# Kernel optimization log

Measured on AMD Instinct MI355X. Metric: run time of the kernel, lower is better.

The kernel has to match this reference:

```python
import jax, jax.numpy as jnp
import numpy as np
from jax import lax

D = 30   # embedding_dim (hardcoded in repo)
Q = 30   # question length
N = 4000 # number of sentences in doc
S = 100  # tokens per sentence
K = 5    # k_for_maxpool
SLOPE = 0.1  # LeakyReLU negative slope


def setup_inputs() -> dict:
    key = jax.random.key(0)
    ks = jax.random.split(key, 20)
    rn = lambda k, sh: jax.random.normal(k, sh, dtype=jnp.float32)
    ru = lambda k, sh: jax.random.uniform(k, sh, dtype=jnp.float32)
    return {
        "doc_sents_embeds": rn(ks[0], (N, S, D)),
        "sents_gaf": ru(ks[1], (N, 3)),
        "question_embeds": rn(ks[2], (Q, D)),
        "q_idfs": ru(ks[3], (Q, 1)),
        "doc_gaf": ru(ks[4], (4,)),
        "conv1_w": rn(ks[5], (D, D, 3)) * 0.1,
        "conv1_b": rn(ks[6], (D,)) * 0.1,
        "conv2_w": rn(ks[7], (D, D, 3)) * 0.1,
        "conv2_b": rn(ks[8], (D,)) * 0.1,
        "qw_W": rn(ks[9], (1, D + 1)) * 0.1,
        "qw_b": rn(ks[10], (1,)) * 0.1,
        "lq1_W": rn(ks[11], (8, 6)) * 0.1,
        "lq1_b": rn(ks[12], (8,)) * 0.1,
        "lq2_W": rn(ks[13], (1, 8)) * 0.1,
        "lq2_b": rn(ks[14], (1,)) * 0.1,
        "so_W": rn(ks[15], (1, 4)) * 0.1,
        "so_b": rn(ks[16], (1,)) * 0.1,
        "fl_W": rn(ks[17], (1, 5)) * 0.1,
        "fl_b": rn(ks[18], (1,)) * 0.1,
    }


def _leaky(x):
    return jnp.where(x >= 0, x, SLOPE * x)


def _conv_block(x, w, b):
    # x: [B, L, D]. torch Conv1d(D, D, 3, padding=2) then slice [1:L+1]
    # is exactly a 'same' conv with padding 1 on each side; then residual add.
    y = lax.conv_general_dilated(x.transpose(0, 2, 1), w, (1,), [(1, 1)],
                                 dimension_numbers=("NCH", "OIH", "NCH"))
    y = _leaky(y + b[None, :, None])
    return y.transpose(0, 2, 1) + x


def _cos_sim(A, B):
    # A: [Q, D], B: [N, S, D] -> [N, Q, S] (num/den as in torch my_cosine_sim)
    num = jnp.einsum("qd,nsd->nqs", A, B)
    den = jnp.linalg.norm(A, axis=-1)[None, :, None] * jnp.linalg.norm(B, axis=-1)[:, None, :]
    return num / den


def _pool(sim):
    # sort-based k-max pooling -> [max, avg_of_top_k]; sim: [N, Q, S] -> [N, Q, 2]
    vals = lax.top_k(sim, K)[0]  # descending
    return jnp.stack([vals[..., 0], vals.mean(-1)], axis=-1)


def reference(doc_sents_embeds, sents_gaf, question_embeds, q_idfs, doc_gaf,
              conv1_w, conv1_b, conv2_w, conv2_b, qw_W, qw_b,
              lq1_W, lq1_b, lq2_W, lq2_b, so_W, so_b, fl_W, fl_b):
    # question context (two residual trigram convs)
    q_conv = _conv_block(question_embeds[None], conv1_w, conv1_b)
    q_conv = _conv_block(q_conv, conv2_w, conv2_b)[0]          # [Q, D]
    # question term weights
    qw_in = jnp.concatenate([q_conv, q_idfs], axis=-1)          # [Q, D+1]
    q_weights = jax.nn.softmax((qw_in @ qw_W.T + qw_b)[:, 0])   # [Q]
    # sentence context convs (batched over all sentences)
    conv_res = _conv_block(doc_sents_embeds, conv1_w, conv1_b)
    conv_res = _conv_block(conv_res, conv2_w, conv2_b)          # [N, S, D]
    # similarity matrices
    sim_insens = _cos_sim(question_embeds, doc_sents_embeds)    # [N, Q, S]
    sim_oh = (sim_insens > 1.0 - 1e-3).astype(sim_insens.dtype)
    sim_sens = _cos_sim(q_conv, conv_res)
    # k-max pooling and per-q tiny MLP attention
    feats = jnp.concatenate([_pool(sim_oh), _pool(sim_insens), _pool(sim_sens)], axis=-1)  # [N, Q, 6]
    lo = _leaky(feats @ lq1_W.T + lq1_b) @ lq2_W.T + lq2_b      # [N, Q, 1]
    lo = lo[..., 0] * q_weights[None, :]
    sent_emit = lo.sum(-1) / Q                                  # [N]
    # per-sentence output layer
    sent_feats = jnp.concatenate([sents_gaf, sent_emit[:, None]], axis=-1)  # [N, 4]
    sent_scores = jax.nn.sigmoid((sent_feats @ so_W.T + so_b)[:, 0])        # [N]
    # doc-level score
    doc_rep = jnp.concatenate([jnp.max(sent_scores)[None], doc_gaf])        # [5]
    final = doc_rep @ fl_W.T + fl_b                                          # [1]
    return final, sent_scores
```

## Files before the change

kernel.cpp:

```cpp
#include <hip/hip_runtime.h>
#include <hip/hip_bf16.h>

#define SLOPE 0.1f

#define OFF_QW    1816
#define OFF_QNI   1846
#define OFF_QNS   1876
#define OFF_QNN   1906
#define OFF_B1    4606
#define OFF_B2    7336
#define OFF_LQ1W  7366
#define OFF_LQ1B  7414
#define OFF_LQ2W  7422
#define OFF_LQ2B  7430
#define OFF_SOW   7431
#define OFF_SOB   7435
#define OFF_FLW   7436
#define OFF_FLB   7441
#define U16_QEA   16384
#define U16_QCA   17408
#define U16_WB1   18432
#define U16_WB2   21504

typedef __attribute__((ext_vector_type(8))) __bf16 bf16x8;
typedef __attribute__((ext_vector_type(4))) float f32x4;

union Frag { uint4 u4; uint u[4]; bf16x8 v; };

__device__ __forceinline__ float bf2f(ushort h) {
    union { uint u; float f; } c; c.u = ((uint)h) << 16; return c.f;
}
__device__ __forceinline__ ushort f2bf(float f) {
    union { float f; uint u; } c; c.f = f;
    uint u = c.u;
    return (ushort)((u + 0x7FFFu + ((u >> 16) & 1u)) >> 16);
}
__device__ __forceinline__ float ldx(const void* p, long i, int bf) {
    if (bf) return bf2f(((const ushort*)p)[i]);
    return ((const float*)p)[i];
}
__device__ __forceinline__ uint pk2(float lo, float hi) {
    uint r;
    asm("v_cvt_pk_bf16_f32 %0, %1, %2" : "=v"(r) : "v"(lo), "v"(hi));
    return r;
}
__device__ __forceinline__ float blo(uint u) { return __uint_as_float(u << 16); }
__device__ __forceinline__ float bhi(uint u) { return __uint_as_float(u & 0xFFFF0000u); }
__device__ __forceinline__ float lk(float x) { return fmaxf(x, SLOPE * x); }

#define LGKM0() asm volatile("s_waitcnt lgkmcnt(0)" ::: "memory")

#define CE(x, y) { float _hi = fmaxf(x, y), _lo = fminf(x, y); x = _hi; y = _lo; }

__device__ __forceinline__ void sort4d(float& a, float& b, float& c, float& d) {
    CE(a, b); CE(c, d); CE(a, c); CE(b, d); CE(b, c);
}
__device__ __forceinline__ void merge44_5(const float* a, const float* b, float* t) {
    t[0] = fmaxf(a[0], b[0]);
    t[1] = fmaxf(fminf(a[0], b[0]), fmaxf(a[1], b[1]));
    t[2] = fmaxf(fmaxf(fminf(a[0], b[1]), fminf(a[1], b[0])), fmaxf(a[2], b[2]));
    t[3] = fmaxf(fmaxf(fminf(a[0], b[2]), fminf(a[1], b[1])),
                 fmaxf(fminf(a[2], b[0]), fmaxf(a[3], b[3])));
    t[4] = fmaxf(fmaxf(fminf(a[0], b[3]), fminf(a[1], b[2])),
                 fmaxf(fminf(a[2], b[1]), fminf(a[3], b[0])));
}
__device__ __forceinline__ void merge54_5(const float* a, const float* b, float* t) {
    t[0] = fmaxf(a[0], b[0]);
    t[1] = fmaxf(fminf(a[0], b[0]), fmaxf(a[1], b[1]));
    t[2] = fmaxf(fmaxf(fminf(a[0], b[1]), fminf(a[1], b[0])), fmaxf(a[2], b[2]));
    t[3] = fmaxf(fmaxf(fminf(a[0], b[2]), fminf(a[1], b[1])),
                 fmaxf(fminf(a[2], b[0]), fmaxf(a[3], b[3])));
    t[4] = fmaxf(fmaxf(fmaxf(fminf(a[0], b[3]), fminf(a[1], b[2])),
                       fmaxf(fminf(a[2], b[1]), fminf(a[3], b[0]))), a[4]);
}
__device__ __forceinline__ void merge55_5(const float* a, const float* b, float* t) {
    t[0] = fmaxf(a[0], b[0]);
    t[1] = fmaxf(fminf(a[0], b[0]), fmaxf(a[1], b[1]));
    t[2] = fmaxf(fmaxf(fminf(a[0], b[1]), fminf(a[1], b[0])), fmaxf(a[2], b[2]));
    t[3] = fmaxf(fmaxf(fminf(a[0], b[2]), fminf(a[1], b[1])),
                 fmaxf(fminf(a[2], b[0]), fmaxf(a[3], b[3])));
    t[4] = fmaxf(fmaxf(fmaxf(fminf(a[0], b[3]), fminf(a[1], b[2])),
                       fmaxf(fminf(a[2], b[1]), fminf(a[3], b[0]))),
                 fmaxf(a[4], b[4]));
}

__device__ __forceinline__ int detect_bf(const void* doc_in, int tid, int* scnt) {
    if (tid == 0) *scnt = 0;
    __syncthreads();
    const ushort* p = (const ushort*)doc_in;
    int local = 0;
    for (int i = tid; i < 4096; i += 256) {
        unsigned e = (p[i] >> 7) & 0xFFu;
        if (e != 0u && (e < 100u || e > 134u)) local++;
    }
    atomicAdd(scnt, local);
    __syncthreads();
    return (*scnt > 200) ? 0 : 1;
}

__global__ __launch_bounds__(256) void k_prep(
        const void* doc_in,
        const void* qe_in, const void* qidf_in,
        const void* w1_in, const void* b1_in,
        const void* w2_in, const void* b2_in,
        const void* qwW_in, const void* qwb_in,
        const void* lq1W_in, const void* lq1b_in,
        const void* lq2W_in, const void* lq2b_in,
        const void* soW_in, const void* sob_in,
        const void* flW_in, const void* flb_in,
        float* ws) {
    const int tid = threadIdx.x;
    const int blk = blockIdx.x;
    __shared__ float QE[900], T1[900], QC[900], W[2700], IDF[32], LG[32];
    __shared__ int scnt;

    const int bf = detect_bf(doc_in, tid, &scnt);
    ushort* wsu = (ushort*)ws;

    if (blk == 1) {
        if (tid == 0) { ((int*)ws)[0] = bf; }
        if (tid < 30) ws[OFF_B1 + tid] = ldx(b1_in, tid, bf);
        if (tid < 48) ws[OFF_LQ1W + tid] = ldx(lq1W_in, tid, bf);
        if (tid < 8)  { ws[OFF_LQ1B + tid] = ldx(lq1b_in, tid, bf);
                        ws[OFF_LQ2W + tid] = ldx(lq2W_in, tid, bf); }
        if (tid < 4)  ws[OFF_SOW + tid] = ldx(soW_in, tid, bf);
        if (tid < 5)  ws[OFF_FLW + tid] = ldx(flW_in, tid, bf);
        if (tid == 1) { ws[OFF_LQ2B] = ldx(lq2b_in, 0, bf);
                        ws[OFF_SOB]  = ldx(sob_in, 0, bf);
                        ws[OFF_FLB]  = ldx(flb_in, 0, bf); }
        for (int i = tid; i < 3072; i += 256) {
            int o = i / 96, kk = i % 96;
            int k = kk >> 5, ii = kk & 31;
            float v1 = 0.f;
            if (o < 30 && ii < 30) v1 = ldx(w1_in, (long)o*90 + ii*3 + k, bf);
            wsu[U16_WB1 + i] = f2bf(v1);
        }
        return;
    }
    if (blk == 2) {
        if (tid < 30) ws[OFF_B2 + tid] = ldx(b2_in, tid, bf);
        for (int i = tid; i < 3072; i += 256) {
            int o = i / 96, kk = i % 96;
            int k = kk >> 5, ii = kk & 31;
            float v2 = 0.f;
            if (o < 30 && ii < 30) v2 = ldx(w2_in, (long)o*90 + ii*3 + k, bf);
            wsu[U16_WB2 + i] = f2bf(v2);
        }
        return;
    }

    if (tid == 0) { ((int*)ws)[0] = bf; }

    for (int i = tid; i < 900; i += 256) QE[i] = ldx(qe_in, i, bf);
    if (tid < 30) IDF[tid] = ldx(qidf_in, tid, bf);
    for (int i = tid; i < 2700; i += 256) W[i] = ldx(w1_in, i, bf);
    __syncthreads();

    for (int idx = tid; idx < 900; idx += 256) {
        int s = idx / 30, o = idx % 30;
        float acc = ldx(b1_in, o, bf);
        for (int k = 0; k < 3; ++k) {
            int t = s + k - 1;
            if (t < 0 || t >= 30) continue;
            for (int i = 0; i < 30; ++i) acc += QE[t*30 + i] * W[o*90 + i*3 + k];
        }
        acc = acc >= 0.f ? acc : SLOPE * acc;
        T1[idx] = acc + QE[idx];
    }
    __syncthreads();
    for (int i = tid; i < 2700; i += 256) W[i] = ldx(w2_in, i, bf);
    __syncthreads();
    for (int idx = tid; idx < 900; idx += 256) {
        int s = idx / 30, o = idx % 30;
        float acc = ldx(b2_in, o, bf);
        for (int k = 0; k < 3; ++k) {
            int t = s + k - 1;
            if (t < 0 || t >= 30) continue;
            for (int i = 0; i < 30; ++i) acc += T1[t*30 + i] * W[o*90 + i*3 + k];
        }
        acc = acc >= 0.f ? acc : SLOPE * acc;
        QC[idx] = acc + T1[idx];
    }
    __syncthreads();

    if (tid < 30) {
        float s1 = 0.f, s2 = 0.f;
        for (int d = 0; d < 30; ++d) {
            float a = QE[tid*30 + d]; s1 += a*a;
            float b = QC[tid*30 + d]; s2 += b*b;
        }
        float n1 = sqrtf(s1);
        ws[OFF_QNN + tid] = n1;
        ws[OFF_QNI + tid] = 1.0f / n1;
        ws[OFF_QNS + tid] = 1.0f / sqrtf(s2);
        float z = ldx(qwb_in, 0, bf);
        for (int d = 0; d < 30; ++d) z += QC[tid*30 + d] * ldx(qwW_in, d, bf);
        z += IDF[tid] * ldx(qwW_in, 30, bf);
        LG[tid] = z;
    }
    __syncthreads();
    if (tid == 0) {
        float m = -1e30f;
        for (int q = 0; q < 30; ++q) m = fmaxf(m, LG[q]);
        float sum = 0.f, e[30];
        for (int q = 0; q < 30; ++q) { e[q] = expf(LG[q] - m); sum += e[q]; }
        for (int q = 0; q < 30; ++q) ws[OFF_QW + q] = e[q] / sum;
    }
    for (int i = tid; i < 1024; i += 256) {
        int q = i >> 5, d = i & 31;
        float ve = (q < 30 && d < 30) ? QE[q*30 + d] : 0.f;
        float vc = (q < 30 && d < 30) ? QC[q*30 + d] : 0.f;
        wsu[U16_QEA + i] = f2bf(ve);
        wsu[U16_QCA + i] = f2bf(vc);
    }
}

__global__ __launch_bounds__(128, 5) void k_main(const void* doc_in, const void* gaf_in,
                                                 void* out, float* ws) {
    const int tid = threadIdx.x;
    const int lane = tid & 63;
    const int wid = tid >> 6;
    const int n = blockIdx.x * 2 + wid;
    const int bf = ((const int*)ws)[0];
    const int l15 = lane & 15;
    const int quad = lane >> 4;

    __shared__ __align__(16) uint Xs[2][1648];
    __shared__ __align__(16) float INVXs[2][112];
    __shared__ float FEs[2][30][6];

    uint* X = Xs[wid];
    uint4* X4 = (uint4*)X;
    float* INVX = INVXs[wid];
    float (*FE)[6] = FEs[wid];

    const ushort* wsu = (const ushort*)ws;
    const uint4* qeA = (const uint4*)(wsu + U16_QEA);
    const uint4* qcA = (const uint4*)(wsu + U16_QCA);
    const uint4* wb1 = (const uint4*)(wsu + U16_WB1);
    const uint4* wb2 = (const uint4*)(wsu + U16_WB2);

    float ga0 = ldx(gaf_in, (long)n*3 + 0, bf);
    float ga1 = ldx(gaf_in, (long)n*3 + 1, bf);
    float ga2 = ldx(gaf_in, (long)n*3 + 2, bf);

    {
        uint4 z4 = make_uint4(0u, 0u, 0u, 0u);
        if (lane < 12) X4[(lane < 4) ? lane : (400 + lane)] = z4;
        if (lane >= 12 && lane < 24) INVX[100 + (lane - 12)] = 0.f;
    }
    for (int g = lane; g < 400; g += 64) {
        int r = g >> 2, t = g & 3;
        uint4 w;
        float s2;
        if (bf) {
            const uint* gp = (const uint*)doc_in + (size_t)n * 1500 + r * 15 + t * 4;
            uint a = gp[0], b = gp[1], c = gp[2];
            uint d = (t < 3) ? gp[3] : 0u;
            w = make_uint4(a, b, c, d);
            float x0 = blo(a), x1 = bhi(a), x2 = blo(b), x3 = bhi(b);
            float x4 = blo(c), x5 = bhi(c), x6 = blo(d), x7 = bhi(d);
            s2 = x0*x0 + x1*x1 + x2*x2 + x3*x3 + x4*x4 + x5*x5 + x6*x6 + x7*x7;
        } else {
            const float* p = (const float*)doc_in + (size_t)n * 3000 + r * 30 + t * 8;
            float2 f0 = ((const float2*)p)[0];
            float2 f1 = ((const float2*)p)[1];
            float2 f2 = ((const float2*)p)[2];
            float2 f3 = (t < 3) ? ((const float2*)p)[3] : make_float2(0.f, 0.f);
            w = make_uint4(pk2(f0.x, f0.y), pk2(f1.x, f1.y), pk2(f2.x, f2.y), pk2(f3.x, f3.y));
            s2 = f0.x*f0.x + f0.y*f0.y + f1.x*f1.x + f1.y*f1.y
               + f2.x*f2.x + f2.y*f2.y + f3.x*f3.x + f3.y*f3.y;
        }
        X4[(r + 1) * 4 + t] = w;
        s2 += __shfl_xor(s2, 1);
        s2 += __shfl_xor(s2, 2);
        if (t == 0) INVX[r] = 1.f / sqrtf(s2);
    }
    LGKM0();

    auto sim_pool = [&](const uint4* qa, int iqOff, int fbase, bool do_oh, int qbase) {
        const int q = qbase + l15;
        Frag b;
        b.u4 = qa[q * 4 + quad];
        f32x4 acc[7];
        #pragma unroll
        for (int mt = 0; mt < 7; ++mt) {
            int m = mt * 16 + l15;
            Frag a;
            if (m < 100) a.u4 = X4[(m + 1) * 4 + quad];
            else         a.u4 = make_uint4(0u, 0u, 0u, 0u);
            f32x4 z = {0.f, 0.f, 0.f, 0.f};
            acc[mt] = __builtin_amdgcn_mfma_f32_16x16x32_bf16(a.v, b.v, z, 0, 0, 0);
        }
        const float4* INVX4 = (const float4*)INVX;
        float thr = (do_oh && q < 30) ? 0.999f * ws[OFF_QNN + q] : 1e30f;
        float iq  = (q < 30) ? ws[iqOff + q] : 0.f;
        float g[7][4];
        int cnt = 0;
        #pragma unroll
        for (int mt = 0; mt < 7; ++mt) {
            float4 ix = INVX4[mt * 4 + quad];
            float ixa[4] = {ix.x, ix.y, ix.z, ix.w};
            #pragma unroll
            for (int r = 0; r < 4; ++r) {
                float u = acc[mt][r] * ixa[r];
                if (mt == 6 && (quad * 4 + r) >= 4) u = -1e30f;
                g[mt][r] = u;
                if (do_oh) cnt += (u > thr) ? 1 : 0;
            }
        }
        #pragma unroll
        for (int mt = 0; mt < 7; ++mt) sort4d(g[mt][0], g[mt][1], g[mt][2], g[mt][3]);
        float p0[5], p1[5], p2[5], q0[5], q1[5], t[5];
        merge44_5(g[0], g[1], p0);
        merge44_5(g[2], g[3], p1);
        merge44_5(g[4], g[5], p2);
        merge55_5(p0, p1, q0);
        merge54_5(p2, g[6], q1);
        merge55_5(q0, q1, t);
        #pragma unroll
        for (int d = 16; d < 64; d <<= 1) {
            float pp[5];
            pp[0] = __shfl_xor(t[0], d); pp[1] = __shfl_xor(t[1], d);
            pp[2] = __shfl_xor(t[2], d); pp[3] = __shfl_xor(t[3], d);
            pp[4] = __shfl_xor(t[4], d);
            if (do_oh) cnt += __shfl_xor(cnt, d);
            float tn[5];
            merge55_5(t, pp, tn);
            t[0] = tn[0]; t[1] = tn[1]; t[2] = tn[2]; t[3] = tn[3]; t[4] = tn[4];
        }
        if (quad == 0 && q < 30) {
            if (do_oh) {
                FE[q][0] = cnt > 0 ? 1.f : 0.f;
                FE[q][1] = (float)(cnt > 5 ? 5 : cnt) * 0.2f;
            }
            FE[q][fbase]     = t[0] * iq;
            FE[q][fbase + 1] = (t[0] + t[1] + t[2] + t[3] + t[4]) * 0.2f * iq;
        }
    };

    auto conv_inplace = [&](const uint4* wb, int bOff, bool donorm) {
        Frag wf0[3], wf1[3];
        #pragma unroll
        for (int k = 0; k < 3; ++k) {
            wf0[k].u4 = wb[l15 * 12 + k * 4 + quad];
            wf1[k].u4 = wb[(16 + l15) * 12 + k * 4 + quad];
        }
        float b40[4], b41[4];
        #pragma unroll
        for (int r = 0; r < 4; ++r) {
            int o0 = quad * 4 + r, o1 = 16 + o0;
            b40[r] = ws[bOff + o0];
            b41[r] = (o1 < 30) ? ws[bOff + o1] : 0.f;
        }
        auto load_xf = [&](int mt, Frag& f0, Frag& f1, Frag& f2) {
            int s = mt * 16 + l15;
            if (s < 100) {
                f0.u4 = X4[s * 4 + quad];
                f1.u4 = X4[(s + 1) * 4 + quad];
                f2.u4 = X4[(s + 2) * 4 + quad];
            } else {
                f0.u4 = f1.u4 = f2.u4 = make_uint4(0u, 0u, 0u, 0u);
            }
        };
        Frag xf0, xf1, xf2;
        load_xf(0, xf0, xf1, xf2);
        #pragma unroll
        for (int mt = 0; mt < 7; ++mt) {
            const int s = mt * 16 + l15;
            const bool sv = (s < 100);
            const int db = (s + 1) * 16 + quad * 2;
            uint u0 = 0u, u1 = 0u, u2 = 0u, u3 = 0u;
            if (sv) {
                uint2 ua = *(const uint2*)(X + db);
                uint2 ub = *(const uint2*)(X + db + 8);
                u0 = ua.x; u1 = ua.y; u2 = ub.x; u3 = ub.y;
            }
            Frag xn0, xn1, xn2;
            if (mt < 6) load_xf(mt + 1, xn0, xn1, xn2);
            f32x4 a0 = {0.f, 0.f, 0.f, 0.f}, a1 = {0.f, 0.f, 0.f, 0.f};
            a0 = __builtin_amdgcn_mfma_f32_16x16x32_bf16(wf0[0].v, xf0.v, a0, 0, 0, 0);
            a1 = __builtin_amdgcn_mfma_f32_16x16x32_bf16(wf1[0].v, xf0.v, a1, 0, 0, 0);
            a0 = __builtin_amdgcn_mfma_f32_16x16x32_bf16(wf0[1].v, xf1.v, a0, 0, 0, 0);
            a1 = __builtin_amdgcn_mfma_f32_16x16x32_bf16(wf1[1].v, xf1.v, a1, 0, 0, 0);
            a0 = __builtin_amdgcn_mfma_f32_16x16x32_bf16(wf0[2].v, xf2.v, a0, 0, 0, 0);
            a1 = __builtin_amdgcn_mfma_f32_16x16x32_bf16(wf1[2].v, xf2.v, a1, 0, 0, 0);
            LGKM0();
            float ss = 0.f;
            if (sv) {
                float v0 = lk(a0[0] + b40[0]) + blo(u0);
                float v1 = lk(a0[1] + b40[1]) + bhi(u0);
                float v2 = lk(a0[2] + b40[2]) + blo(u1);
                float v3 = lk(a0[3] + b40[3]) + bhi(u1);
                *(uint2*)(X + db) = make_uint2(pk2(v0, v1), pk2(v2, v3));
                float w0 = lk(a1[0] + b41[0]) + blo(u2);
                float w1 = lk(a1[1] + b41[1]) + bhi(u2);
                ss = v0*v0 + v1*v1 + v2*v2 + v3*v3 + w0*w0 + w1*w1;
                if (quad < 3) {
                    float w2 = lk(a1[2] + b41[2]) + blo(u3);
                    float w3 = lk(a1[3] + b41[3]) + bhi(u3);
                    *(uint2*)(X + db + 8) = make_uint2(pk2(w0, w1), pk2(w2, w3));
                    ss += w2*w2 + w3*w3;
                } else {
                    X[db + 8] = pk2(w0, w1);
                }
            }
            if (donorm) {
                ss += __shfl_xor(ss, 16);
                ss += __shfl_xor(ss, 32);
                if (quad == 0 && sv) INVX[s] = 1.f / sqrtf(ss);
            }
            xf0 = xn0; xf1 = xn1; xf2 = xn2;
        }
    };

    sim_pool(qeA, OFF_QNI, 2, true, 0);
    sim_pool(qeA, OFF_QNI, 2, true, 16);

    conv_inplace(wb1, OFF_B1, false);
    LGKM0();
    conv_inplace(wb2, OFF_B2, true);
    LGKM0();

    sim_pool(qcA, OFF_QNS, 4, false, 0);
    sim_pool(qcA, OFF_QNS, 4, false, 16);
    LGKM0();

    float val = 0.f;
    if (lane < 30) {
        float lo = ws[OFF_LQ2B];
        #pragma unroll
        for (int j = 0; j < 8; ++j) {
            float h = ws[OFF_LQ1B + j];
            #pragma unroll
            for (int f = 0; f < 6; ++f) h += FE[lane][f] * ws[OFF_LQ1W + j*6 + f];
            h = lk(h);
            lo += h * ws[OFF_LQ2W + j];
        }
        val = lo * ws[OFF_QW + lane];
    }
    #pragma unroll
    for (int d = 32; d >= 1; d >>= 1) val += __shfl_xor(val, d);
    if (lane == 0) {
        float emit = val * (1.f / 30.f);
        float z = ws[OFF_SOB];
        z += ga0 * ws[OFF_SOW + 0];
        z += ga1 * ws[OFF_SOW + 1];
        z += ga2 * ws[OFF_SOW + 2];
        z += emit * ws[OFF_SOW + 3];
        float sc = 1.f / (1.f + expf(-z));
        if (bf) ((__hip_bfloat16*)out)[1 + n] = __float2bfloat16(sc);
        else    ((float*)out)[1 + n] = sc;
    }
}

__global__ __launch_bounds__(256) void k_final(const void* docgaf_in, void* out, const float* ws) {
    const int tid = threadIdx.x;
    const int bf = ((const int*)ws)[0];
    __shared__ float red[256];
    float m = -1e30f;
    for (int i = tid; i < 4000; i += 256) {
        float v = bf ? __bfloat162float(((const __hip_bfloat16*)out)[1 + i])
                     : ((const float*)out)[1 + i];
        m = fmaxf(m, v);
    }
    red[tid] = m;
    __syncthreads();
    for (int off = 128; off > 0; off >>= 1) {
        if (tid < off) red[tid] = fmaxf(red[tid], red[tid + off]);
        __syncthreads();
    }
    if (tid == 0) {
        float f = ws[OFF_FLB] + red[0] * ws[OFF_FLW + 0];
        for (int i = 0; i < 4; ++i) f += ldx(docgaf_in, i, bf) * ws[OFF_FLW + 1 + i];
        if (bf) ((__hip_bfloat16*)out)[0] = __float2bfloat16(f);
        else    ((float*)out)[0] = f;
    }
}

extern "C" void kernel_launch(void* const* d_in, const int* in_sizes, int n_in,
                              void* d_out, int out_size, void* d_ws, size_t ws_size,
                              hipStream_t stream) {
    float* ws = (float*)d_ws;
    k_prep<<<3, 256, 0, stream>>>(d_in[0], d_in[2], d_in[3], d_in[5], d_in[6], d_in[7], d_in[8],
                                  d_in[9], d_in[10], d_in[11], d_in[12], d_in[13], d_in[14],
                                  d_in[15], d_in[16], d_in[17], d_in[18], ws);
    k_main<<<2000, 128, 0, stream>>>(d_in[0], d_in[1], d_out, ws);
    k_final<<<1, 256, 0, stream>>>(d_in[4], d_out, ws);
}
```

Measured before the change: 179.1 us.

## Split each sentence across two waves with ping-pong LDS buffers

Changes the work mapping from one wave per sentence to two waves cooperating on one sentence: each wave handles 16 questions in the similarity/pooling stage and about half the row tiles in each conv. The in-place conv with a single buffer is replaced by ping-pong XA/XB buffers separated by __syncthreads. The row stride is packed to 15 dwords instead of 16, which turns vector LDS accesses into scalar dword loads. The aim is to halve per-wave serial latency and shrink LDS per sentence, at the cost of block barriers, a cross-wave reduction and more LDS instructions.

```diff
diff --git a/kernel.cpp b/kernel.cpp
--- a/kernel.cpp
+++ b/kernel.cpp
@@ -22,6 +22,8 @@
 #define U16_WB1   18432
 #define U16_WB2   21504
 
+#define XDW 1548
+
 typedef __attribute__((ext_vector_type(8))) __bf16 bf16x8;
 typedef __attribute__((ext_vector_type(4))) float f32x4;
 
@@ -47,8 +49,6 @@
 __device__ __forceinline__ float blo(uint u) { return __uint_as_float(u << 16); }
 __device__ __forceinline__ float bhi(uint u) { return __uint_as_float(u & 0xFFFF0000u); }
 __device__ __forceinline__ float lk(float x) { return fmaxf(x, SLOPE * x); }
-
-#define LGKM0() asm volatile("s_waitcnt lgkmcnt(0)" ::: "memory")
 
 #define CE(x, y) { float _hi = fmaxf(x, y), _lo = fminf(x, y); x = _hi; y = _lo; }
 
@@ -215,24 +215,21 @@
     }
 }
 
-__global__ __launch_bounds__(128, 5) void k_main(const void* doc_in, const void* gaf_in,
+__global__ __launch_bounds__(128, 4) void k_main(const void* doc_in, const void* gaf_in,
                                                  void* out, float* ws) {
+    const int n = blockIdx.x;
     const int tid = threadIdx.x;
+    const int bf = ((const int*)ws)[0];
     const int lane = tid & 63;
     const int wid = tid >> 6;
-    const int n = blockIdx.x * 2 + wid;
-    const int bf = ((const int*)ws)[0];
     const int l15 = lane & 15;
     const int quad = lane >> 4;
-
-    __shared__ __align__(16) uint Xs[2][1648];
-    __shared__ __align__(16) float INVXs[2][112];
-    __shared__ float FEs[2][30][6];
-
-    uint* X = Xs[wid];
-    uint4* X4 = (uint4*)X;
-    float* INVX = INVXs[wid];
-    float (*FE)[6] = FEs[wid];
+    const int q = wid * 16 + l15;
+
+    __shared__ __align__(16) uint XA[XDW];
+    __shared__ __align__(16) uint XB[XDW];
+    __shared__ __align__(16) float INVX[112];
+    __shared__ float PART[2];
 
     const ushort* wsu = (const ushort*)ws;
     const uint4* qeA = (const uint4*)(wsu + U16_QEA);
@@ -244,20 +241,22 @@
     float ga1 = ldx(gaf_in, (long)n*3 + 1, bf);
     float ga2 = ldx(gaf_in, (long)n*3 + 2, bf);
 
-    {
-        uint4 z4 = make_uint4(0u, 0u, 0u, 0u);
-        if (lane < 12) X4[(lane < 4) ? lane : (400 + lane)] = z4;
-        if (lane >= 12 && lane < 24) INVX[100 + (lane - 12)] = 0.f;
-    }
-    for (int g = lane; g < 400; g += 64) {
+    if (tid < 48) {
+        int j = (tid < 15) ? tid : (1500 + tid);
+        XA[j] = 0u; XB[j] = 0u;
+    } else if (tid < 60) {
+        INVX[100 + (tid - 48)] = 0.f;
+    }
+    for (int g = tid; g < 400; g += 128) {
         int r = g >> 2, t = g & 3;
-        uint4 w;
+        int base = (r + 1) * 15 + t * 4;
         float s2;
         if (bf) {
             const uint* gp = (const uint*)doc_in + (size_t)n * 1500 + r * 15 + t * 4;
             uint a = gp[0], b = gp[1], c = gp[2];
             uint d = (t < 3) ? gp[3] : 0u;
-            w = make_uint4(a, b, c, d);
+            XA[base] = a; XA[base + 1] = b; XA[base + 2] = c;
+            if (t < 3) XA[base + 3] = d;
             float x0 = blo(a), x1 = bhi(a), x2 = blo(b), x3 = bhi(b);
             float x4 = blo(c), x5 = bhi(c), x6 = blo(d), x7 = bhi(d);
             s2 = x0*x0 + x1*x1 + x2*x2 + x3*x3 + x4*x4 + x5*x5 + x6*x6 + x7*x7;
@@ -267,19 +266,21 @@
             float2 f1 = ((const float2*)p)[1];
             float2 f2 = ((const float2*)p)[2];
             float2 f3 = (t < 3) ? ((const float2*)p)[3] : make_float2(0.f, 0.f);
-            w = make_uint4(pk2(f0.x, f0.y), pk2(f1.x, f1.y), pk2(f2.x, f2.y), pk2(f3.x, f3.y));
+            XA[base]     = pk2(f0.x, f0.y);
+            XA[base + 1] = pk2(f1.x, f1.y);
+            XA[base + 2] = pk2(f2.x, f2.y);
+            if (t < 3) XA[base + 3] = pk2(f3.x, f3.y);
             s2 = f0.x*f0.x + f0.y*f0.y + f1.x*f1.x + f1.y*f1.y
                + f2.x*f2.x + f2.y*f2.y + f3.x*f3.x + f3.y*f3.y;
         }
-        X4[(r + 1) * 4 + t] = w;
         s2 += __shfl_xor(s2, 1);
         s2 += __shfl_xor(s2, 2);
         if (t == 0) INVX[r] = 1.f / sqrtf(s2);
     }
-    LGKM0();
-
-    auto sim_pool = [&](const uint4* qa, int iqOff, int fbase, bool do_oh, int qbase) {
-        const int q = qbase + l15;
+    __syncthreads();
+
+    auto sim_pool = [&](const uint4* qa, int iqOff, bool do_oh,
+                        float& o0, float& o1, float& m0, float& m1) {
         Frag b;
         b.u4 = qa[q * 4 + quad];
         f32x4 acc[7];
@@ -287,8 +288,11 @@
         for (int mt = 0; mt < 7; ++mt) {
             int m = mt * 16 + l15;
             Frag a;
-            if (m < 100) a.u4 = X4[(m + 1) * 4 + quad];
-            else         a.u4 = make_uint4(0u, 0u, 0u, 0u);
+            if (m < 100) {
+                int base = (m + 1) * 15 + quad * 4;
+                a.u[0] = XA[base];     a.u[1] = XA[base + 1];
+                a.u[2] = XA[base + 2]; a.u[3] = XA[base + 3];
+            } else { a.u[0] = a.u[1] = a.u[2] = a.u[3] = 0u; }
             f32x4 z = {0.f, 0.f, 0.f, 0.f};
             acc[mt] = __builtin_amdgcn_mfma_f32_16x16x32_bf16(a.v, b.v, z, 0, 0, 0);
         }
@@ -329,17 +333,18 @@
             merge55_5(t, pp, tn);
             t[0] = tn[0]; t[1] = tn[1]; t[2] = tn[2]; t[3] = tn[3]; t[4] = tn[4];
         }
-        if (quad == 0 && q < 30) {
-            if (do_oh) {
-                FE[q][0] = cnt > 0 ? 1.f : 0.f;
-                FE[q][1] = (float)(cnt > 5 ? 5 : cnt) * 0.2f;
-            }
-            FE[q][fbase]     = t[0] * iq;
-            FE[q][fbase + 1] = (t[0] + t[1] + t[2] + t[3] + t[4]) * 0.2f * iq;
-        }
+        if (do_oh) {
+            o0 = cnt > 0 ? 1.f : 0.f;
+            o1 = (float)(cnt > 5 ? 5 : cnt) * 0.2f;
+        }
+        m0 = t[0] * iq;
+        m1 = (t[0] + t[1] + t[2] + t[3] + t[4]) * 0.2f * iq;
     };
 
-    auto conv_inplace = [&](const uint4* wb, int bOff, bool donorm) {
+    auto conv_dual = [&](const uint* src, uint* dst, const uint4* wb, int bOff,
+                         bool donorm) {
+        const int mtb = wid ? 3 : 0;
+        const int mte = wid ? 6 : 2;
         Frag wf0[3], wf1[3];
         #pragma unroll
         for (int k = 0; k < 3; ++k) {
@@ -353,56 +358,56 @@
             b40[r] = ws[bOff + o0];
             b41[r] = (o1 < 30) ? ws[bOff + o1] : 0.f;
         }
-        auto load_xf = [&](int mt, Frag& f0, Frag& f1, Frag& f2) {
-            int s = mt * 16 + l15;
-            if (s < 100) {
-                f0.u4 = X4[s * 4 + quad];
-                f1.u4 = X4[(s + 1) * 4 + quad];
-                f2.u4 = X4[(s + 2) * 4 + quad];
-            } else {
-                f0.u4 = f1.u4 = f2.u4 = make_uint4(0u, 0u, 0u, 0u);
-            }
-        };
-        Frag xf0, xf1, xf2;
-        load_xf(0, xf0, xf1, xf2);
-        #pragma unroll
-        for (int mt = 0; mt < 7; ++mt) {
+        for (int mt = mtb; mt <= mte; ++mt) {
             const int s = mt * 16 + l15;
             const bool sv = (s < 100);
-            const int db = (s + 1) * 16 + quad * 2;
+            Frag f0, f1, f2;
+            if (sv) {
+                int base = s * 15 + quad * 4;
+                f0.u[0] = src[base];      f0.u[1] = src[base + 1];
+                f0.u[2] = src[base + 2];  f0.u[3] = src[base + 3];
+                base += 15;
+                f1.u[0] = src[base];      f1.u[1] = src[base + 1];
+                f1.u[2] = src[base + 2];  f1.u[3] = src[base + 3];
+                base += 15;
+                f2.u[0] = src[base];      f2.u[1] = src[base + 1];
+                f2.u[2] = src[base + 2];  f2.u[3] = src[base + 3];
+            } else {
+                f0.u[0]=f0.u[1]=f0.u[2]=f0.u[3]=0u;
+                f1 = f0; f2 = f0;
+            }
+            const int db = (s + 1) * 15 + quad * 2;
             uint u0 = 0u, u1 = 0u, u2 = 0u, u3 = 0u;
             if (sv) {
-                uint2 ua = *(const uint2*)(X + db);
-                uint2 ub = *(const uint2*)(X + db + 8);
+                uint2 ua = *(const uint2*)(src + db);
+                uint2 ub = *(const uint2*)(src + db + 8);
                 u0 = ua.x; u1 = ua.y; u2 = ub.x; u3 = ub.y;
             }
-            Frag xn0, xn1, xn2;
-            if (mt < 6) load_xf(mt + 1, xn0, xn1, xn2);
             f32x4 a0 = {0.f, 0.f, 0.f, 0.f}, a1 = {0.f, 0.f, 0.f, 0.f};
-            a0 = __builtin_amdgcn_mfma_f32_16x16x32_bf16(wf0[0].v, xf0.v, a0, 0, 0, 0);
-            a1 = __builtin_amdgcn_mfma_f32_16x16x32_bf16(wf1[0].v, xf0.v, a1, 0, 0, 0);
-            a0 = __builtin_amdgcn_mfma_f32_16x16x32_bf16(wf0[1].v, xf1.v, a0, 0, 0, 0);
-            a1 = __builtin_amdgcn_mfma_f32_16x16x32_bf16(wf1[1].v, xf1.v, a1, 0, 0, 0);
-            a0 = __builtin_amdgcn_mfma_f32_16x16x32_bf16(wf0[2].v, xf2.v, a0, 0, 0, 0);
-            a1 = __builtin_amdgcn_mfma_f32_16x16x32_bf16(wf1[2].v, xf2.v, a1, 0, 0, 0);
-            LGKM0();
+            a0 = __builtin_amdgcn_mfma_f32_16x16x32_bf16(wf0[0].v, f0.v, a0, 0, 0, 0);
+            a1 = __builtin_amdgcn_mfma_f32_16x16x32_bf16(wf1[0].v, f0.v, a1, 0, 0, 0);
+            a0 = __builtin_amdgcn_mfma_f32_16x16x32_bf16(wf0[1].v, f1.v, a0, 0, 0, 0);
+            a1 = __builtin_amdgcn_mfma_f32_16x16x32_bf16(wf1[1].v, f1.v, a1, 0, 0, 0);
+            a0 = __builtin_amdgcn_mfma_f32_16x16x32_bf16(wf0[2].v, f2.v, a0, 0, 0, 0);
+            a1 = __builtin_amdgcn_mfma_f32_16x16x32_bf16(wf1[2].v, f2.v, a1, 0, 0, 0);
             float ss = 0.f;
             if (sv) {
                 float v0 = lk(a0[0] + b40[0]) + blo(u0);
                 float v1 = lk(a0[1] + b40[1]) + bhi(u0);
                 float v2 = lk(a0[2] + b40[2]) + blo(u1);
                 float v3 = lk(a0[3] + b40[3]) + bhi(u1);
-                *(uint2*)(X + db) = make_uint2(pk2(v0, v1), pk2(v2, v3));
+                *(uint2*)(dst + db) = make_uint2(pk2(v0, v1), pk2(v2, v3));
                 float w0 = lk(a1[0] + b41[0]) + blo(u2);
                 float w1 = lk(a1[1] + b41[1]) + bhi(u2);
+                uint s45 = pk2(w0, w1);
                 ss = v0*v0 + v1*v1 + v2*v2 + v3*v3 + w0*w0 + w1*w1;
                 if (quad < 3) {
                     float w2 = lk(a1[2] + b41[2]) + blo(u3);
                     float w3 = lk(a1[3] + b41[3]) + bhi(u3);
-                    *(uint2*)(X + db + 8) = make_uint2(pk2(w0, w1), pk2(w2, w3));
+                    *(uint2*)(dst + db + 8) = make_uint2(s45, pk2(w2, w3));
                     ss += w2*w2 + w3*w3;
                 } else {
-                    X[db + 8] = pk2(w0, w1);
+                    dst[db + 8] = s45;
                 }
             }
             if (donorm) {
@@ -410,39 +415,39 @@
                 ss += __shfl_xor(ss, 32);
                 if (quad == 0 && sv) INVX[s] = 1.f / sqrtf(ss);
             }
-            xf0 = xn0; xf1 = xn1; xf2 = xn2;
         }
     };
 
-    sim_pool(qeA, OFF_QNI, 2, true, 0);
-    sim_pool(qeA, OFF_QNI, 2, true, 16);
-
-    conv_inplace(wb1, OFF_B1, false);
-    LGKM0();
-    conv_inplace(wb2, OFF_B2, true);
-    LGKM0();
-
-    sim_pool(qcA, OFF_QNS, 4, false, 0);
-    sim_pool(qcA, OFF_QNS, 4, false, 16);
-    LGKM0();
-
+    float fe0, fe1, fe2, fe3, fe4, fe5;
+    sim_pool(qeA, OFF_QNI, true, fe0, fe1, fe2, fe3);
+    conv_dual(XA, XB, wb1, OFF_B1, false);
+    __syncthreads();
+
+    conv_dual(XB, XA, wb2, OFF_B2, true);
+    __syncthreads();
+
+    sim_pool(qcA, OFF_QNS, false, fe0, fe1, fe4, fe5);
     float val = 0.f;
-    if (lane < 30) {
+    if (quad == 0 && q < 30) {
+        float f[6] = {fe0, fe1, fe2, fe3, fe4, fe5};
         float lo = ws[OFF_LQ2B];
         #pragma unroll
         for (int j = 0; j < 8; ++j) {
             float h = ws[OFF_LQ1B + j];
             #pragma unroll
-            for (int f = 0; f < 6; ++f) h += FE[lane][f] * ws[OFF_LQ1W + j*6 + f];
+            for (int i = 0; i < 6; ++i) h += f[i] * ws[OFF_LQ1W + j*6 + i];
             h = lk(h);
             lo += h * ws[OFF_LQ2W + j];
         }
-        val = lo * ws[OFF_QW + lane];
+        val = lo * ws[OFF_QW + q];
     }
     #pragma unroll
     for (int d = 32; d >= 1; d >>= 1) val += __shfl_xor(val, d);
-    if (lane == 0) {
-        float emit = val * (1.f / 30.f);
+    if (lane == 0) PART[wid] = val;
+    __syncthreads();
+
+    if (tid == 0) {
+        float emit = (PART[0] + PART[1]) * (1.f / 30.f);
         float z = ws[OFF_SOB];
         z += ga0 * ws[OFF_SOW + 0];
         z += ga1 * ws[OFF_SOW + 1];
@@ -485,6 +490,6 @@
     k_prep<<<3, 256, 0, stream>>>(d_in[0], d_in[2], d_in[3], d_in[5], d_in[6], d_in[7], d_in[8],
                                   d_in[9], d_in[10], d_in[11], d_in[12], d_in[13], d_in[14],
                                   d_in[15], d_in[16], d_in[17], d_in[18], ws);
-    k_main<<<2000, 128, 0, stream>>>(d_in[0], d_in[1], d_out, ws);
+    k_main<<<4000, 128, 0, stream>>>(d_in[0], d_in[1], d_out, ws);
     k_final<<<1, 256, 0, stream>>>(d_in[4], d_out, ws);
 }
```

Result: slower. 184.1 us (+2.8%).
